# Kernel tuning notes

Measured on AMD Instinct MI355X. Metric: run time of the kernel, lower is better.

The kernel has to match this reference:

```python
import jax, jax.numpy as jnp
import numpy as np

EPS = 1e-5  # torch BatchNorm1d default eps


def _batchnorm(x, gamma, beta):
    # training-mode BatchNorm1d: biased batch statistics over the N dim
    mean = jnp.mean(x, axis=0)
    var = jnp.var(x, axis=0)
    return (x - mean) * jax.lax.rsqrt(var + EPS) * gamma + beta


def setup_inputs() -> dict:
    key = jax.random.key(0)
    ks = jax.random.split(key, 12)
    N_last, N_cur, E, F = 100000, 50000, 500000, 300
    Din = F + 3  # 303: neighbor features concat coord delta
    inp = {
        "last_coors": jax.random.normal(ks[0], (N_last, 3), jnp.float32),
        "last_features": jax.random.normal(ks[1], (N_last, F), jnp.float32),
        "current_coors": jax.random.normal(ks[2], (N_cur, 3), jnp.float32),
        "cur_idx": jax.random.randint(ks[3], (E,), 0, N_cur),
        "last_idx": jax.random.randint(ks[4], (E,), 0, N_last),
        # in_linear: Linear(303,300) + ReLU + BN(300)
        "W1": jax.random.normal(ks[5], (Din, F), jnp.float32) / np.sqrt(Din),
        "b1": jnp.zeros((F,), jnp.float32),
        "g1": jnp.ones((F,), jnp.float32),
        "be1": jnp.zeros((F,), jnp.float32),
        # out_linear: Linear(300,300) + ReLU + BN(300)
        "W2": jax.random.normal(ks[6], (F, F), jnp.float32) / np.sqrt(F),
        "b2": jnp.zeros((F,), jnp.float32),
        "g2": jnp.ones((F,), jnp.float32),
        "be2": jnp.zeros((F,), jnp.float32),
    }
    return inp


def reference(last_coors, last_features, current_coors, cur_idx, last_idx,
              W1, b1, g1, be1, W2, b2, g2, be2):
    N_cur = current_coors.shape[0]
    # gather: neighbor features + (neighbor - center) coordinate deltas -> [E, 303]
    edge_feats = jnp.concatenate(
        [last_features[last_idx], last_coors[last_idx] - current_coors[cur_idx]],
        axis=1)
    # in_linear MLP on edges
    h = _batchnorm(jnp.maximum(edge_feats @ W1 + b1, 0.0), g1, be1)  # [E, 300]
    # scatter-max aggregation to current-level nodes (empty segments -> 0,
    # matching torch_scatter.scatter(..., reduce='max') zero-init behavior)
    agg = jax.ops.segment_max(h, cur_idx, num_segments=N_cur)  # [N_cur, 300]
    agg = jnp.where(jnp.isfinite(agg), agg, 0.0)
    # out_linear MLP on nodes
    out = _batchnorm(jnp.maximum(agg @ W2 + b2, 0.0), g2, be2)
    return out
```

## Files before the change

kernel.cpp:

```cpp
#include <hip/hip_runtime.h>
#include <hip/hip_bf16.h>


#define NPART 64
#define SB 256
#define SEGB 32
#define CHS 256
#define UNR 8

typedef __bf16 bf16_t;
typedef __bf16 bf16x8 __attribute__((ext_vector_type(8)));
typedef float f32x4 __attribute__((ext_vector_type(4)));

__global__ void hist_k(const int* __restrict__ ci, int E, int* __restrict__ hist)
{
    const int e = blockIdx.x * 256 + threadIdx.x;
    if (e < E) atomicAdd(&hist[ci[e]], 1);
}

__global__ void scan_reduce(const int* __restrict__ hist, int nseg, int* __restrict__ bsum)
{
    __shared__ int s[SB];
    const int tid = threadIdx.x;
    const int i = blockIdx.x * SB + tid;
    s[tid] = (i < nseg) ? hist[i] : 0;
    __syncthreads();
    for (int o = SB / 2; o > 0; o >>= 1) {
        if (tid < o) s[tid] += s[tid + o];
        __syncthreads();
    }
    if (tid == 0) bsum[blockIdx.x] = s[0];
}

__global__ void scan_top(int* __restrict__ bsum, int nb)
{
    __shared__ int s[SB];
    const int tid = threadIdx.x;
    const int v = (tid < nb) ? bsum[tid] : 0;
    s[tid] = v;
    __syncthreads();
    for (int o = 1; o < SB; o <<= 1) {
        int x = 0;
        if (tid >= o) x = s[tid - o];
        __syncthreads();
        s[tid] += x;
        __syncthreads();
    }
    if (tid < nb) bsum[tid] = s[tid] - v;
}

__global__ void scan_final(const int* __restrict__ hist, int nseg,
                           const int* __restrict__ bsum, int* __restrict__ cnt)
{
    __shared__ int s[SB];
    const int tid = threadIdx.x;
    const int i = blockIdx.x * SB + tid;
    const int v = (i < nseg) ? hist[i] : 0;
    s[tid] = v;
    __syncthreads();
    for (int o = 1; o < SB; o <<= 1) {
        int x = 0;
        if (tid >= o) x = s[tid - o];
        __syncthreads();
        s[tid] += x;
        __syncthreads();
    }
    if (i < nseg) cnt[i] = s[tid] - v + bsum[blockIdx.x];
}

__global__ void scatter_k(const int* __restrict__ ci, const int* __restrict__ li,
                          int E, int* __restrict__ cnt, int2* __restrict__ sorted)
{
    const int e = blockIdx.x * 256 + threadIdx.x;
    if (e >= E) return;
    const int c = ci[e];
    const int pos = atomicAdd(&cnt[c], 1);
    sorted[pos] = make_int2(li[e], c);
}

__global__ void pack_wt2(const float* __restrict__ W1, const float* __restrict__ W2,
                         bf16_t* __restrict__ WT)
{
    const int idx = blockIdx.x * 256 + threadIdx.x;
    if (idx >= 2 * 384 * 320) return;
    const int w = idx / (384 * 320);
    const int rem = idx - w * (384 * 320);
    const int n = rem / 320, k = rem % 320;
    const float* W = w ? W2 : W1;
    float v = (n < 300 && k < 300) ? W[k * 300 + n] : 0.f;
    WT[idx] = (bf16_t)v;
}

template<int MODE>
__launch_bounds__(256)
__global__ void gemm_mfma(const float* __restrict__ A32, int M,
                          const int* __restrict__ segEnd,
                          const float* __restrict__ ac,
                          const bf16_t* __restrict__ WT,
                          const float* __restrict__ bias,
                          bf16_t* __restrict__ outBF,
                          float* __restrict__ outF,
                          float* __restrict__ part)
{
    __shared__ bf16_t As[128][72];
    __shared__ bf16_t Bs[160][72];
    __shared__ float sSum[160], sSq[160];

    const int tid  = threadIdx.x;
    const int lane = tid & 63, wv = tid >> 6;
    const int wm = wv & 1, wn = wv >> 1;
    const int m0 = blockIdx.x * 128, n0 = blockIdx.y * 160;
    const int rl = lane & 15, quad = lane >> 4;

    if (MODE == 1 && tid < 160) { sSum[tid] = 0.f; sSq[tid] = 0.f; }

    f32x4 acc[4][5];
    #pragma unroll
    for (int i = 0; i < 4; ++i)
        #pragma unroll
        for (int j = 0; j < 5; ++j)
            acc[i][j] = (f32x4){0.f, 0.f, 0.f, 0.f};

    for (int k0 = 0; k0 < 320; k0 += 64) {
        #pragma unroll
        for (int i = 0; i < 4; ++i) {
            const int id = i * 256 + tid;
            const int r = id >> 3, kc = (id & 7) * 8;
            const int gr = min(m0 + r, M - 1);
            const int c0 = k0 + kc;
            bf16x8 v = {};
            if (MODE == 0) {
                if (c0 + 8 <= 300) {
                    const float4 a = *reinterpret_cast<const float4*>(&A32[(long)gr * 300 + c0]);
                    const float4 b = *reinterpret_cast<const float4*>(&A32[(long)gr * 300 + c0 + 4]);
                    v = (bf16x8){(bf16_t)a.x, (bf16_t)a.y, (bf16_t)a.z, (bf16_t)a.w,
                                 (bf16_t)b.x, (bf16_t)b.y, (bf16_t)b.z, (bf16_t)b.w};
                } else if (c0 < 300) {
                    const float4 a = *reinterpret_cast<const float4*>(&A32[(long)gr * 300 + c0]);
                    v[0] = (bf16_t)a.x; v[1] = (bf16_t)a.y;
                    v[2] = (bf16_t)a.z; v[3] = (bf16_t)a.w;
                }
            } else {
                const bool emp = segEnd[gr] == (gr ? segEnd[gr - 1] : 0);
                const float4 ma = *reinterpret_cast<const float4*>(&A32[(long)gr * 320 + c0]);
                const float4 mb = *reinterpret_cast<const float4*>(&A32[(long)gr * 320 + c0 + 4]);
                const float4 aa = *reinterpret_cast<const float4*>(&ac[c0]);
                const float4 ab = *reinterpret_cast<const float4*>(&ac[c0 + 4]);
                const float4 ca = *reinterpret_cast<const float4*>(&ac[320 + c0]);
                const float4 cb = *reinterpret_cast<const float4*>(&ac[320 + c0 + 4]);
                const float t0 = emp ? 0.f : fabsf(aa.x) * ma.x + ca.x;
                const float t1 = emp ? 0.f : fabsf(aa.y) * ma.y + ca.y;
                const float t2 = emp ? 0.f : fabsf(aa.z) * ma.z + ca.z;
                const float t3 = emp ? 0.f : fabsf(aa.w) * ma.w + ca.w;
                const float t4 = emp ? 0.f : fabsf(ab.x) * mb.x + cb.x;
                const float t5 = emp ? 0.f : fabsf(ab.y) * mb.y + cb.y;
                const float t6 = emp ? 0.f : fabsf(ab.z) * mb.z + cb.z;
                const float t7 = emp ? 0.f : fabsf(ab.w) * mb.w + cb.w;
                v = (bf16x8){(bf16_t)t0, (bf16_t)t1, (bf16_t)t2, (bf16_t)t3,
                             (bf16_t)t4, (bf16_t)t5, (bf16_t)t6, (bf16_t)t7};
            }
            *reinterpret_cast<bf16x8*>(&As[r][kc]) = v;
        }
        #pragma unroll
        for (int i = 0; i < 5; ++i) {
            const int id = i * 256 + tid;
            const int n = id >> 3, kc = (id & 7) * 8;
            bf16x8 w8 = *reinterpret_cast<const bf16x8*>(&WT[(long)(n0 + n) * 320 + k0 + kc]);
            *reinterpret_cast<bf16x8*>(&Bs[n][kc]) = w8;
        }
        __syncthreads();

        #pragma unroll
        for (int kk = 0; kk < 2; ++kk) {
            const int kb = kk * 32 + quad * 8;
            bf16x8 af[4], bfr[5];
            #pragma unroll
            for (int mi = 0; mi < 4; ++mi)
                af[mi] = *reinterpret_cast<const bf16x8*>(&As[wm * 64 + mi * 16 + rl][kb]);
            #pragma unroll
            for (int nj = 0; nj < 5; ++nj)
                bfr[nj] = *reinterpret_cast<const bf16x8*>(&Bs[wn * 80 + nj * 16 + rl][kb]);
            #pragma unroll
            for (int mi = 0; mi < 4; ++mi)
                #pragma unroll
                for (int nj = 0; nj < 5; ++nj)
                    acc[mi][nj] = __builtin_amdgcn_mfma_f32_16x16x32_bf16(
                        af[mi], bfr[nj], acc[mi][nj], 0, 0, 0);
        }
        __syncthreads();
    }

    if (MODE == 0) {
        #pragma unroll
        for (int mi = 0; mi < 4; ++mi)
            #pragma unroll
            for (int nj = 0; nj < 5; ++nj)
                #pragma unroll
                for (int reg = 0; reg < 4; ++reg) {
                    const int r = m0 + wm * 64 + mi * 16 + quad * 4 + reg;
                    const int c = n0 + wn * 80 + nj * 16 + rl;
                    if (r < M) {
                        const float v = (c < 300) ? (acc[mi][nj][reg] + bias[c]) : 0.f;
                        outBF[(long)r * 320 + c] = (bf16_t)v;
                    }
                }
    } else {
        float csum[5] = {}, csq[5] = {};
        #pragma unroll
        for (int mi = 0; mi < 4; ++mi)
            #pragma unroll
            for (int nj = 0; nj < 5; ++nj)
                #pragma unroll
                for (int reg = 0; reg < 4; ++reg) {
                    const int r = m0 + wm * 64 + mi * 16 + quad * 4 + reg;
                    const int c = n0 + wn * 80 + nj * 16 + rl;
                    if (r < M && c < 300) {
                        float v = fmaxf(acc[mi][nj][reg] + bias[c], 0.f);
                        outF[(long)r * 300 + c] = v;
                        csum[nj] += v; csq[nj] += v * v;
                    }
                }
        #pragma unroll
        for (int nj = 0; nj < 5; ++nj) {
            const int cl = wn * 80 + nj * 16 + rl;
            atomicAdd(&sSum[cl], csum[nj]);
            atomicAdd(&sSq[cl], csq[nj]);
        }
        __syncthreads();
        const int slot = (blockIdx.x + blockIdx.y * gridDim.x) & (NPART - 1);
        if (tid < 160 && (n0 + tid) < 300) {
            atomicAdd(&part[slot * 600 + n0 + tid], sSum[tid]);
            atomicAdd(&part[slot * 600 + 300 + n0 + tid], sSq[tid]);
        }
    }
}

__launch_bounds__(320)
__global__ void edge_pass(const bf16_t* __restrict__ Gb,
                          const float* __restrict__ last_coors,
                          const float* __restrict__ cur_coors,
                          const int2* __restrict__ sorted,
                          const int*  __restrict__ segEnd,
                          const float* __restrict__ Wc,
                          const float* __restrict__ g1,
                          float* __restrict__ zbuf,
                          float* __restrict__ part1,
                          int N_cur)
{
    __shared__ int sRow[2][CHS], sCi[2][CHS];
    __shared__ float sD0[2][CHS], sD1[2][CHS], sD2[2][CHS];

    const int tid = threadIdx.x;
    const int st  = (tid >= 160) ? 1 : 0;
    const int ts  = tid - st * 160;

    const int g0   = blockIdx.x * SEGB;
    const int gEnd = min(g0 + SEGB, N_cur);
    const int gMid = min(g0 + SEGB / 2, gEnd);

    const int e00 = (g0   == 0) ? 0 : segEnd[g0 - 1];
    const int e01 = (gMid == 0) ? 0 : segEnd[gMid - 1];
    const int e11 = (gEnd == 0) ? 0 : segEnd[gEnd - 1];

    const int ebeg = st ? e01 : e00;
    const int eend = st ? e11 : e01;

    const int nch0 = (e01 - e00 + CHS - 1) / CHS;
    const int nch1 = (e11 - e01 + CHS - 1) / CHS;
    const int nch  = max(nch0, nch1);

    const int ft = ts * 2;
    const bool real = (ft < 300);
    float w00 = 0.f, w01 = 0.f, w10 = 0.f, w11 = 0.f, w20 = 0.f, w21 = 0.f;
    float sgn0 = 1.f, sgn1 = 1.f;
    if (real) {
        w00 = Wc[ft];        w01 = Wc[ft + 1];
        w10 = Wc[300 + ft];  w11 = Wc[300 + ft + 1];
        w20 = Wc[600 + ft];  w21 = Wc[600 + ft + 1];
        sgn0 = (g1[ft]     < 0.f) ? -1.f : 1.f;
        sgn1 = (g1[ft + 1] < 0.f) ? -1.f : 1.f;
    }

    int cur = -1;
    float m0 = -3.4e38f, m1 = -3.4e38f;
    float sum0 = 0.f, sq0 = 0.f, sum1 = 0.f, sq1 = 0.f;

    for (int ch = 0; ch < nch; ++ch) {
        const int cbeg = ebeg + ch * CHS;
        const int ccnt = min(CHS, eend - cbeg);

        for (int i = ts; i < ccnt; i += 160) {
            const int2 r = sorted[cbeg + i];
            sRow[st][i] = r.x * 320;
            sCi[st][i]  = r.y;
            sD0[st][i] = last_coors[r.x * 3 + 0] - cur_coors[r.y * 3 + 0];
            sD1[st][i] = last_coors[r.x * 3 + 1] - cur_coors[r.y * 3 + 1];
            sD2[st][i] = last_coors[r.x * 3 + 2] - cur_coors[r.y * 3 + 2];
        }
        __syncthreads();

        int i = 0;
        for (; i + UNR <= ccnt; i += UNR) {
            unsigned gu[UNR];
            #pragma unroll
            for (int j = 0; j < UNR; ++j)
                gu[j] = *reinterpret_cast<const unsigned*>(&Gb[(long)sRow[st][i + j] + ft]);
            #pragma unroll
            for (int j = 0; j < UNR; ++j) {
                const int ci = sCi[st][i + j];
                if (ci != cur) {
                    if (cur >= 0)
                        *reinterpret_cast<float2*>(&zbuf[(long)cur * 320 + ft]) =
                            make_float2(m0, m1);
                    cur = ci;
                    m0 = -3.4e38f; m1 = -3.4e38f;
                }
                const float gx = __uint_as_float(gu[j] << 16);
                const float gy = __uint_as_float(gu[j] & 0xffff0000u);
                const float d0 = sD0[st][i + j], d1 = sD1[st][i + j], d2 = sD2[st][i + j];
                const float y0 = fmaxf(gx + d0 * w00 + d1 * w10 + d2 * w20, 0.f);
                const float y1 = fmaxf(gy + d0 * w01 + d1 * w11 + d2 * w21, 0.f);
                sum0 += y0; sq0 += y0 * y0; m0 = fmaxf(m0, sgn0 * y0);
                sum1 += y1; sq1 += y1 * y1; m1 = fmaxf(m1, sgn1 * y1);
            }
        }
        for (; i < ccnt; ++i) {
            const int ci = sCi[st][i];
            if (ci != cur) {
                if (cur >= 0)
                    *reinterpret_cast<float2*>(&zbuf[(long)cur * 320 + ft]) =
                        make_float2(m0, m1);
                cur = ci;
                m0 = -3.4e38f; m1 = -3.4e38f;
            }
            const unsigned gu = *reinterpret_cast<const unsigned*>(&Gb[(long)sRow[st][i] + ft]);
            const float gx = __uint_as_float(gu << 16);
            const float gy = __uint_as_float(gu & 0xffff0000u);
            const float d0 = sD0[st][i], d1 = sD1[st][i], d2 = sD2[st][i];
            const float y0 = fmaxf(gx + d0 * w00 + d1 * w10 + d2 * w20, 0.f);
            const float y1 = fmaxf(gy + d0 * w01 + d1 * w11 + d2 * w21, 0.f);
            sum0 += y0; sq0 += y0 * y0; m0 = fmaxf(m0, sgn0 * y0);
            sum1 += y1; sq1 += y1 * y1; m1 = fmaxf(m1, sgn1 * y1);
        }
        __syncthreads();
    }
    if (cur >= 0)
        *reinterpret_cast<float2*>(&zbuf[(long)cur * 320 + ft]) = make_float2(m0, m1);

    const int slot = blockIdx.x & (NPART - 1);
    if (real) {
        atomicAdd(&part1[slot * 600 + ft],           sum0);
        atomicAdd(&part1[slot * 600 + ft + 1],       sum1);
        atomicAdd(&part1[slot * 600 + 300 + ft],     sq0);
        atomicAdd(&part1[slot * 600 + 300 + ft + 1], sq1);
    }
}

__global__ void stats_finalize(const float* __restrict__ part,
                               const float* __restrict__ g,
                               const float* __restrict__ be,
                               float invCnt, float* __restrict__ ac)
{
    const int t = threadIdx.x;
    if (t >= 300) {
        if (t < 320) { ac[t] = 0.f; ac[320 + t] = 0.f; }
        return;
    }
    float sum = 0.f, sq = 0.f;
    for (int p = 0; p < NPART; ++p) {
        sum += part[p * 600 + t];
        sq  += part[p * 600 + 300 + t];
    }
    const float mean = sum * invCnt;
    const float var = fmaxf(sq * invCnt - mean * mean, 0.f);
    const float inv = rsqrtf(var + 1e-5f);
    const float a = g[t] * inv;
    ac[t] = a;
    ac[320 + t] = be[t] - mean * a;
}

__global__ void finalize_out(float* __restrict__ out,
                             const float* __restrict__ ac2)
{
    const int t = threadIdx.x;
    if (t >= 300) return;
    const long i = (long)blockIdx.x * 300 + t;
    out[i] = ac2[t] * out[i] + ac2[320 + t];
}

extern "C" void kernel_launch(void* const* d_in, const int* in_sizes, int n_in,
                              void* d_out, int out_size, void* d_ws, size_t ws_size,
                              hipStream_t stream)
{
    const float* last_coors    = (const float*)d_in[0];
    const float* last_features = (const float*)d_in[1];
    const float* cur_coors     = (const float*)d_in[2];
    const int*   cur_idx       = (const int*)d_in[3];
    const int*   last_idx      = (const int*)d_in[4];
    const float* W1  = (const float*)d_in[5];
    const float* b1  = (const float*)d_in[6];
    const float* g1  = (const float*)d_in[7];
    const float* be1 = (const float*)d_in[8];
    const float* W2  = (const float*)d_in[9];
    const float* b2  = (const float*)d_in[10];
    const float* g2  = (const float*)d_in[11];
    const float* be2 = (const float*)d_in[12];
    float* out = (float*)d_out;

    const int N_last = in_sizes[0] / 3;
    const int N_cur  = in_sizes[2] / 3;
    const int E      = in_sizes[3];

    const int nb1 = (N_cur + SB - 1) / SB;

    char* ws = (char*)d_ws;
    size_t off = 0;
    bf16_t* Gb = (bf16_t*)(ws + off);  off += (size_t)N_last * 320 * 2;
    off = (off + 255) & ~(size_t)255;
    float* zbuf = (float*)(ws + off);  off += (size_t)N_cur * 320 * 4;
    off = (off + 255) & ~(size_t)255;
    int2* sorted = (int2*)(ws + off);  off += (size_t)E * 8;
    int* hist = (int*)(ws + off);      off += (size_t)nb1 * SB * 4;
    int* cnt  = (int*)(ws + off);      off += (size_t)nb1 * SB * 4;
    int* bsum = (int*)(ws + off);      off += 256 * 4;
    bf16_t* WT1 = (bf16_t*)(ws + off); off += (size_t)384 * 320 * 2;
    bf16_t* WT2 = (bf16_t*)(ws + off); off += (size_t)384 * 320 * 2;
    float* part1 = (float*)(ws + off); off += (size_t)NPART * 600 * 4;
    float* part2 = (float*)(ws + off); off += (size_t)NPART * 600 * 4;
    float* ac1   = (float*)(ws + off); off += 640 * 4;
    float* ac2   = (float*)(ws + off); off += 640 * 4;

    hipMemsetAsync(hist, 0, (size_t)nb1 * SB * 4, stream);
    hipMemsetAsync(part1, 0, (size_t)2 * NPART * 600 * 4, stream);

    hist_k<<<(E + 255) / 256, 256, 0, stream>>>(cur_idx, E, hist);
    scan_reduce<<<nb1, SB, 0, stream>>>(hist, N_cur, bsum);
    scan_top<<<1, SB, 0, stream>>>(bsum, nb1);
    scan_final<<<nb1, SB, 0, stream>>>(hist, N_cur, bsum, cnt);
    scatter_k<<<(E + 255) / 256, 256, 0, stream>>>(cur_idx, last_idx, E, cnt, sorted);

    pack_wt2<<<960, 256, 0, stream>>>(W1, W2, WT1);

    dim3 gridG((N_last + 127) / 128, 2);
    gemm_mfma<0><<<gridG, 256, 0, stream>>>(last_features, N_last, nullptr, nullptr,
                                            WT1, b1, Gb, nullptr, nullptr);

    const int nSB = (N_cur + SEGB - 1) / SEGB;
    edge_pass<<<nSB, 320, 0, stream>>>(Gb, last_coors, cur_coors, sorted, cnt,
                                       W1 + 300 * 300, g1, zbuf, part1, N_cur);

    stats_finalize<<<1, 320, 0, stream>>>(part1, g1, be1, 1.0f / (float)E, ac1);

    dim3 grid2((N_cur + 127) / 128, 2);
    gemm_mfma<1><<<grid2, 256, 0, stream>>>(zbuf, N_cur, cnt, ac1,
                                            WT2, b2, nullptr, out, part2);

    stats_finalize<<<1, 320, 0, stream>>>(part2, g2, be2, 1.0f / (float)N_cur, ac2);
    finalize_out<<<N_cur, 320, 0, stream>>>(out, ac2);
}
```

Before: 587.9 us.

## Read GEMM weight fragments directly from global, drop B LDS tile, swap grid order

The GEMM kernel stops staging the weight tile in shared memory. Each wave now loads its B fragments straight from the small, cache-resident packed weight buffer, which removes half the LDS traffic and shrinks the LDS footprint. Gathered row indices and empty-segment flags are hoisted out of the K loop, and all A loads are issued before conversion to improve memory-level parallelism. The grid is transposed so the two N-tiles of the same rows run adjacently and share A in cache, and launch bounds request 4 blocks per CU. The trade-off is that B fragments now come from uncoalesced global/L2 reads at MFMA time, and the register cap may cause spills.

New measurement: 626.7 us. +6.6%, slower.

```diff
diff --git a/kernel.cpp b/kernel.cpp
--- a/kernel.cpp
+++ b/kernel.cpp
@@ -92,7 +92,7 @@
 }
 
 template<int MODE>
-__launch_bounds__(256)
+__launch_bounds__(256, 4)
 __global__ void gemm_mfma(const float* __restrict__ A32, int M,
                           const int* __restrict__ segEnd,
                           const float* __restrict__ ac,
@@ -103,16 +103,26 @@
                           float* __restrict__ part)
 {
     __shared__ bf16_t As[128][72];
-    __shared__ bf16_t Bs[160][72];
     __shared__ float sSum[160], sSq[160];
 
     const int tid  = threadIdx.x;
     const int lane = tid & 63, wv = tid >> 6;
     const int wm = wv & 1, wn = wv >> 1;
-    const int m0 = blockIdx.x * 128, n0 = blockIdx.y * 160;
+    const int m0 = blockIdx.y * 128, n0 = blockIdx.x * 160;
     const int rl = lane & 15, quad = lane >> 4;
 
     if (MODE == 1 && tid < 160) { sSum[tid] = 0.f; sSq[tid] = 0.f; }
+
+    const int kcT = (tid & 7) * 8;
+    const int rT  = tid >> 3;
+    int grow[4]; bool emp[4];
+    #pragma unroll
+    for (int i = 0; i < 4; ++i) {
+        grow[i] = min(m0 + i * 32 + rT, M - 1);
+        emp[i] = false;
+        if (MODE == 1)
+            emp[i] = segEnd[grow[i]] == (grow[i] ? segEnd[grow[i] - 1] : 0);
+    }
 
     f32x4 acc[4][5];
     #pragma unroll
@@ -122,51 +132,51 @@
             acc[i][j] = (f32x4){0.f, 0.f, 0.f, 0.f};
 
     for (int k0 = 0; k0 < 320; k0 += 64) {
+        const int c0 = k0 + kcT;
+
+        float4 la[4], lb[4];
+        float4 aa, ab, ca, cb;
+        if (MODE == 1) {
+            aa = *reinterpret_cast<const float4*>(&ac[c0]);
+            ab = *reinterpret_cast<const float4*>(&ac[c0 + 4]);
+            ca = *reinterpret_cast<const float4*>(&ac[320 + c0]);
+            cb = *reinterpret_cast<const float4*>(&ac[320 + c0 + 4]);
+        }
         #pragma unroll
         for (int i = 0; i < 4; ++i) {
-            const int id = i * 256 + tid;
-            const int r = id >> 3, kc = (id & 7) * 8;
-            const int gr = min(m0 + r, M - 1);
-            const int c0 = k0 + kc;
-            bf16x8 v = {};
+            la[i] = make_float4(0.f, 0.f, 0.f, 0.f);
+            lb[i] = make_float4(0.f, 0.f, 0.f, 0.f);
             if (MODE == 0) {
                 if (c0 + 8 <= 300) {
-                    const float4 a = *reinterpret_cast<const float4*>(&A32[(long)gr * 300 + c0]);
-                    const float4 b = *reinterpret_cast<const float4*>(&A32[(long)gr * 300 + c0 + 4]);
-                    v = (bf16x8){(bf16_t)a.x, (bf16_t)a.y, (bf16_t)a.z, (bf16_t)a.w,
-                                 (bf16_t)b.x, (bf16_t)b.y, (bf16_t)b.z, (bf16_t)b.w};
+                    la[i] = *reinterpret_cast<const float4*>(&A32[(long)grow[i] * 300 + c0]);
+                    lb[i] = *reinterpret_cast<const float4*>(&A32[(long)grow[i] * 300 + c0 + 4]);
                 } else if (c0 < 300) {
-                    const float4 a = *reinterpret_cast<const float4*>(&A32[(long)gr * 300 + c0]);
-                    v[0] = (bf16_t)a.x; v[1] = (bf16_t)a.y;
-                    v[2] = (bf16_t)a.z; v[3] = (bf16_t)a.w;
+                    la[i] = *reinterpret_cast<const float4*>(&A32[(long)grow[i] * 300 + c0]);
                 }
             } else {
-                const bool emp = segEnd[gr] == (gr ? segEnd[gr - 1] : 0);
-                const float4 ma = *reinterpret_cast<const float4*>(&A32[(long)gr * 320 + c0]);
-                const float4 mb = *reinterpret_cast<const float4*>(&A32[(long)gr * 320 + c0 + 4]);
-                const float4 aa = *reinterpret_cast<const float4*>(&ac[c0]);
-                const float4 ab = *reinterpret_cast<const float4*>(&ac[c0 + 4]);
-                const float4 ca = *reinterpret_cast<const float4*>(&ac[320 + c0]);
-                const float4 cb = *reinterpret_cast<const float4*>(&ac[320 + c0 + 4]);
-                const float t0 = emp ? 0.f : fabsf(aa.x) * ma.x + ca.x;
-                const float t1 = emp ? 0.f : fabsf(aa.y) * ma.y + ca.y;
-                const float t2 = emp ? 0.f : fabsf(aa.z) * ma.z + ca.z;
-                const float t3 = emp ? 0.f : fabsf(aa.w) * ma.w + ca.w;
-                const float t4 = emp ? 0.f : fabsf(ab.x) * mb.x + cb.x;
-                const float t5 = emp ? 0.f : fabsf(ab.y) * mb.y + cb.y;
-                const float t6 = emp ? 0.f : fabsf(ab.z) * mb.z + cb.z;
-                const float t7 = emp ? 0.f : fabsf(ab.w) * mb.w + cb.w;
+                la[i] = *reinterpret_cast<const float4*>(&A32[(long)grow[i] * 320 + c0]);
+                lb[i] = *reinterpret_cast<const float4*>(&A32[(long)grow[i] * 320 + c0 + 4]);
+            }
+        }
+        #pragma unroll
+        for (int i = 0; i < 4; ++i) {
+            bf16x8 v;
+            if (MODE == 0) {
+                v = (bf16x8){(bf16_t)la[i].x, (bf16_t)la[i].y, (bf16_t)la[i].z, (bf16_t)la[i].w,
+                             (bf16_t)lb[i].x, (bf16_t)lb[i].y, (bf16_t)lb[i].z, (bf16_t)lb[i].w};
+            } else {
+                const float t0 = emp[i] ? 0.f : fabsf(aa.x) * la[i].x + ca.x;
+                const float t1 = emp[i] ? 0.f : fabsf(aa.y) * la[i].y + ca.y;
+                const float t2 = emp[i] ? 0.f : fabsf(aa.z) * la[i].z + ca.z;
+                const float t3 = emp[i] ? 0.f : fabsf(aa.w) * la[i].w + ca.w;
+                const float t4 = emp[i] ? 0.f : fabsf(ab.x) * lb[i].x + cb.x;
+                const float t5 = emp[i] ? 0.f : fabsf(ab.y) * lb[i].y + cb.y;
+                const float t6 = emp[i] ? 0.f : fabsf(ab.z) * lb[i].z + cb.z;
+                const float t7 = emp[i] ? 0.f : fabsf(ab.w) * lb[i].w + cb.w;
                 v = (bf16x8){(bf16_t)t0, (bf16_t)t1, (bf16_t)t2, (bf16_t)t3,
                              (bf16_t)t4, (bf16_t)t5, (bf16_t)t6, (bf16_t)t7};
             }
-            *reinterpret_cast<bf16x8*>(&As[r][kc]) = v;
-        }
-        #pragma unroll
-        for (int i = 0; i < 5; ++i) {
-            const int id = i * 256 + tid;
-            const int n = id >> 3, kc = (id & 7) * 8;
-            bf16x8 w8 = *reinterpret_cast<const bf16x8*>(&WT[(long)(n0 + n) * 320 + k0 + kc]);
-            *reinterpret_cast<bf16x8*>(&Bs[n][kc]) = w8;
+            *reinterpret_cast<bf16x8*>(&As[i * 32 + rT][kcT]) = v;
         }
         __syncthreads();
 
@@ -175,11 +185,12 @@
             const int kb = kk * 32 + quad * 8;
             bf16x8 af[4], bfr[5];
             #pragma unroll
+            for (int nj = 0; nj < 5; ++nj)
+                bfr[nj] = *reinterpret_cast<const bf16x8*>(
+                    &WT[(long)(n0 + wn * 80 + nj * 16 + rl) * 320 + k0 + kb]);
+            #pragma unroll
             for (int mi = 0; mi < 4; ++mi)
                 af[mi] = *reinterpret_cast<const bf16x8*>(&As[wm * 64 + mi * 16 + rl][kb]);
-            #pragma unroll
-            for (int nj = 0; nj < 5; ++nj)
-                bfr[nj] = *reinterpret_cast<const bf16x8*>(&Bs[wn * 80 + nj * 16 + rl][kb]);
             #pragma unroll
             for (int mi = 0; mi < 4; ++mi)
                 #pragma unroll
@@ -441,7 +452,7 @@
 
     pack_wt2<<<960, 256, 0, stream>>>(W1, W2, WT1);
 
-    dim3 gridG((N_last + 127) / 128, 2);
+    dim3 gridG(2, (N_last + 127) / 128);
     gemm_mfma<0><<<gridG, 256, 0, stream>>>(last_features, N_last, nullptr, nullptr,
                                             WT1, b1, Gb, nullptr, nullptr);
 
@@ -451,7 +462,7 @@
 
     stats_finalize<<<1, 320, 0, stream>>>(part1, g1, be1, 1.0f / (float)E, ac1);
 
-    dim3 grid2((N_cur + 127) / 128, 2);
+    dim3 grid2(2, (N_cur + 127) / 128);
     gemm_mfma<1><<<grid2, 256, 0, stream>>>(zbuf, N_cur, cnt, ac1,
                                             WT2, b2, nullptr, out, part2);
 
```
